# Kernel optimization log

Hardware: AMD Instinct MI355X
Metric: run time of the kernel (lower is better)

Reference implementation:

```python
import jax, jax.numpy as jnp
import numpy as np
import math

DIM_IN = 512
DIM_OUT = 512
KERNEL = 3
STYLE_DIM = 2 * 128
LIN_SCALE = 1.0 / math.sqrt(STYLE_DIM)      # EqualLinear scale (lr_mul=1)
CONV_SCALE = 1.0 / math.sqrt(DIM_IN * KERNEL ** 2)  # fan_in = dim_in * k**2 (as in source)
PAD = KERNEL // 2


def setup_inputs() -> dict:
    key = jax.random.key(0)
    ks = jax.random.split(key, 5)
    B, T = 16, 2048
    x = jax.random.normal(ks[0], (B, DIM_IN, T), dtype=jnp.float32)
    c_src = jax.random.normal(ks[1], (B, 128), dtype=jnp.float32)
    c_trg = jax.random.normal(ks[2], (B, 128), dtype=jnp.float32)
    style_w = jax.random.normal(ks[3], (DIM_IN, STYLE_DIM), dtype=jnp.float32)
    style_b = jnp.ones((DIM_IN,), dtype=jnp.float32)  # bias_init=1
    weight = jax.random.normal(ks[4], (1, DIM_OUT, DIM_IN, KERNEL), dtype=jnp.float32)
    return {"x": x, "c_src": c_src, "c_trg": c_trg,
            "style_w": style_w, "style_b": style_b, "weight": weight}


def reference(x, c_src, c_trg, style_w, style_b, weight):
    B = x.shape[0]
    # EqualLinear: style code s [B, dim_in]
    c = jnp.concatenate([c_src, c_trg], axis=-1)              # [B, 256]
    s = c @ (style_w * LIN_SCALE).T + style_b                 # [B, dim_in]
    # Modulate: w [B, dim_out, dim_in, k]
    w = CONV_SCALE * weight * s[:, None, :, None]
    # Demodulate over (dim_in, k)
    demod = jax.lax.rsqrt(jnp.sum(w * w, axis=(2, 3)) + 1e-8)  # [B, dim_out]
    w = w * demod[:, :, None, None]
    # Per-sample conv1d, padding 'same' (pad = k//2), vmapped over batch
    def conv1(xi, wi):
        # xi: [dim_in, T], wi: [dim_out, dim_in, k]
        out = jax.lax.conv_general_dilated(
            xi[None], wi, window_strides=(1,), padding=[(PAD, PAD)],
            dimension_numbers=("NCH", "OIH", "NCH"))
        return out[0]                                          # [dim_out, T]
    return jax.vmap(conv1)(x, w)                               # [B, dim_out, T]
```

## Files before the change

kernel.cpp:

```cpp
#include <hip/hip_runtime.h>
#include <cstdint>
#include <cstddef>


#define LIN_SCALE  0.0625f
#define CONV_SCALE 0.014731391f

#define B_   16
#define CIN  512
#define COUT 512
#define T_   2048
#define TP   2050

typedef __bf16 bf16x8 __attribute__((ext_vector_type(8)));
typedef float  f32x4  __attribute__((ext_vector_type(4)));

__device__ inline unsigned short f2bf(float f) {
  __bf16 h = (__bf16)f;
  return __builtin_bit_cast(unsigned short, h);
}

__global__ void style_kernel(const float* __restrict__ c_src,
                             const float* __restrict__ c_trg,
                             const float* __restrict__ sw,
                             const float* __restrict__ sb,
                             float* __restrict__ s) {
  __shared__ float c[256];
  const int b = blockIdx.x;
  const int tid = threadIdx.x;
  if (tid < 128)       c[tid] = c_src[b * 128 + tid];
  else if (tid < 256)  c[tid] = c_trg[b * 128 + tid - 128];
  __syncthreads();
  float acc = 0.f;
  const float* row = sw + (size_t)tid * 256;
  #pragma unroll 8
  for (int j = 0; j < 256; ++j) acc += row[j] * c[j];
  s[b * 512 + tid] = acc * LIN_SCALE + sb[tid];
}

__global__ __launch_bounds__(256) void modw_kernel(const float* __restrict__ weight,
                                                   const float* __restrict__ s,
                                                   unsigned short* __restrict__ Wm) {
  const int o = blockIdx.x, b = blockIdx.y;
  const int tid = threadIdx.x;
  __shared__ float sv[512];
  __shared__ float red[5];
  sv[tid]       = s[b * 512 + tid];
  sv[tid + 256] = s[b * 512 + tid + 256];
  __syncthreads();

  const float* wrow = weight + (size_t)o * 1536 + tid * 6;
  const int i0 = 2 * tid;
  float v[6]; float ss = 0.f;
  #pragma unroll
  for (int q = 0; q < 6; ++q) {
    const int i = i0 + (q >= 3);
    const float w = wrow[q] * CONV_SCALE * sv[i];
    v[q] = w; ss += w * w;
  }
  #pragma unroll
  for (int off = 32; off > 0; off >>= 1) ss += __shfl_down(ss, off, 64);
  if ((tid & 63) == 0) red[tid >> 6] = ss;
  __syncthreads();
  if (tid == 0) red[4] = rsqrtf(red[0] + red[1] + red[2] + red[3] + 1e-8f);
  __syncthreads();
  const float dem = red[4];

  #pragma unroll
  for (int q = 0; q < 6; ++q) {
    const int i = i0 + (q >= 3);
    const int k = (q >= 3) ? (q - 3) : q;
    Wm[(((size_t)b * 3 + k) * 512 + o) * 512 + i] = f2bf(v[q] * dem);
  }
}

__global__ __launch_bounds__(256) void transpose_kernel(const float* __restrict__ x,
                                                        unsigned short* __restrict__ xT) {
  __shared__ float tile[64][65];
  const int b = blockIdx.z, i0 = blockIdx.y * 64, t0 = blockIdx.x * 64;
  const int c  = threadIdx.x & 63;
  const int r0 = threadIdx.x >> 6;
  const float* xb = x + ((size_t)b * CIN + i0) * T_ + t0;
  #pragma unroll
  for (int rr = 0; rr < 64; rr += 4) {
    const int r = rr + r0;
    tile[r][c] = xb[(size_t)r * T_ + c];
  }
  __syncthreads();
  unsigned short* xTb = xT + ((size_t)b * TP + 1 + t0) * CIN + i0;
  #pragma unroll
  for (int rr = 0; rr < 64; rr += 4) {
    const int t = rr + r0;
    xTb[(size_t)t * CIN + c] = f2bf(tile[c][t]);
  }
}

__global__ void zpad_kernel(unsigned short* __restrict__ xT) {
  const int b = blockIdx.x;
  const size_t base = (size_t)b * TP * CIN;
  for (int j = threadIdx.x; j < CIN; j += 256) {
    xT[base + j] = 0;
    xT[base + (size_t)(TP - 1) * CIN + j] = 0;
  }
}

#define BM 128
#define BN 128
#define BK 64

__global__ __launch_bounds__(256, 2) void gemm_kernel(const unsigned short* __restrict__ Wm,
                                                      const unsigned short* __restrict__ xT,
                                                      float* __restrict__ out) {
  __shared__ unsigned short lA[BM * BK];
  __shared__ unsigned short lB[BN * BK];

  const int b  = blockIdx.z;
  const int o0 = blockIdx.y * BM;
  const int t0 = blockIdx.x * BN;
  const int tid  = threadIdx.x;
  const int lane = tid & 63;
  const int wm = (threadIdx.x >> 6 & 1) * 64;
  const int wn = (threadIdx.x >> 7) * 64;

  const int srow = tid >> 3;
  const int scol = (tid & 7) * 8;
  const unsigned short* gW = Wm + (size_t)b * 3 * 512 * 512 + (size_t)(o0 + srow) * 512 + scol;
  const unsigned short* gX = xT + (size_t)b * TP * CIN + (size_t)(t0 + srow) * CIN + scol;
  unsigned short* lAp = &lA[tid * 8];
  unsigned short* lBp = &lB[tid * 8];

  f32x4 acc[4][4];
  #pragma unroll
  for (int i = 0; i < 4; ++i)
    #pragma unroll
    for (int j = 0; j < 4; ++j) acc[i][j] = (f32x4){0.f, 0.f, 0.f, 0.f};

  for (int kk = 0; kk < 24; ++kk) {
    const int tap = kk >> 3;
    const int i0  = (kk & 7) * 64;
    const size_t offA = (size_t)tap * 512 * 512 + i0;
    const size_t offX = (size_t)tap * CIN + i0;
    __syncthreads();
    #pragma unroll
    for (int p = 0; p < 4; ++p)
      __builtin_amdgcn_global_load_lds(
          (const __attribute__((address_space(1))) void*)(gW + offA + (size_t)p * 32 * 512),
          (__attribute__((address_space(3))) void*)(lAp + p * 2048), 16, 0, 0);
    #pragma unroll
    for (int p = 0; p < 4; ++p)
      __builtin_amdgcn_global_load_lds(
          (const __attribute__((address_space(1))) void*)(gX + offX + (size_t)p * 32 * CIN),
          (__attribute__((address_space(3))) void*)(lBp + p * 2048), 16, 0, 0);
    __syncthreads();

    #pragma unroll
    for (int s = 0; s < 2; ++s) {
      const int ko = s * 32 + (lane >> 4) * 8;
      bf16x8 af[4], bfr[4];
      #pragma unroll
      for (int mi = 0; mi < 4; ++mi)
        af[mi] = *(const bf16x8*)&lA[(wm + mi * 16 + (lane & 15)) * BK + ko];
      #pragma unroll
      for (int ni = 0; ni < 4; ++ni)
        bfr[ni] = *(const bf16x8*)&lB[(wn + ni * 16 + (lane & 15)) * BK + ko];
      #pragma unroll
      for (int mi = 0; mi < 4; ++mi)
        #pragma unroll
        for (int ni = 0; ni < 4; ++ni)
          acc[mi][ni] = __builtin_amdgcn_mfma_f32_16x16x32_bf16(af[mi], bfr[ni], acc[mi][ni], 0, 0, 0);
    }
  }

  float* ob = out + ((size_t)b * COUT + o0 + wm) * T_ + t0 + wn;
  const int rrow = (lane >> 4) * 4;
  const int ccol = lane & 15;
  #pragma unroll
  for (int mi = 0; mi < 4; ++mi)
    #pragma unroll
    for (int ni = 0; ni < 4; ++ni)
      #pragma unroll
      for (int r = 0; r < 4; ++r)
        ob[(size_t)(mi * 16 + rrow + r) * T_ + ni * 16 + ccol] = acc[mi][ni][r];
}

extern "C" void kernel_launch(void* const* d_in, const int* in_sizes, int n_in,
                              void* d_out, int out_size, void* d_ws, size_t ws_size,
                              hipStream_t stream) {
  const float* x       = (const float*)d_in[0];
  const float* c_src   = (const float*)d_in[1];
  const float* c_trg   = (const float*)d_in[2];
  const float* style_w = (const float*)d_in[3];
  const float* style_b = (const float*)d_in[4];
  const float* weight  = (const float*)d_in[5];
  float* out = (float*)d_out;

  char* ws = (char*)d_ws;
  float* s_buf          = (float*)ws;
  unsigned short* Wm    = (unsigned short*)(ws + 32768);
  unsigned short* xTbuf = (unsigned short*)(ws + 32768 + 25165824);

  style_kernel<<<dim3(B_), 512, 0, stream>>>(c_src, c_trg, style_w, style_b, s_buf);
  modw_kernel<<<dim3(COUT, B_), 256, 0, stream>>>(weight, s_buf, Wm);
  transpose_kernel<<<dim3(T_ / 64, CIN / 64, B_), 256, 0, stream>>>(x, xTbuf);
  zpad_kernel<<<dim3(B_), 256, 0, stream>>>(xTbuf);
  gemm_kernel<<<dim3(T_ / BN, COUT / BM, B_), 256, 0, stream>>>(Wm, xTbuf, out);
}
```

Before: 211.9 us.

## Vectorize transpose, batch modulation across samples, parallelize style, raise GEMM occupancy

The style linear is spread over more blocks, with one wavefront reduction per output row. The modulation kernel now loads each weight row once and processes all 16 batch samples in that block, writing bf16 pairs. The transpose uses float4 loads and 16-byte bf16 stores, replacing scalar 2-byte stores. The GEMM launch bound is raised to 4 blocks per CU, which may force register spilling of the 64-float accumulator set.

```diff
diff --git a/kernel.cpp b/kernel.cpp
--- a/kernel.cpp
+++ b/kernel.cpp
@@ -14,63 +14,94 @@
 
 typedef __bf16 bf16x8 __attribute__((ext_vector_type(8)));
 typedef float  f32x4  __attribute__((ext_vector_type(4)));
+typedef unsigned short u16x8 __attribute__((ext_vector_type(8)));
+typedef unsigned short u16x2 __attribute__((ext_vector_type(2)));
 
 __device__ inline unsigned short f2bf(float f) {
   __bf16 h = (__bf16)f;
   return __builtin_bit_cast(unsigned short, h);
 }
 
-__global__ void style_kernel(const float* __restrict__ c_src,
-                             const float* __restrict__ c_trg,
-                             const float* __restrict__ sw,
-                             const float* __restrict__ sb,
-                             float* __restrict__ s) {
+__global__ __launch_bounds__(256) void style_kernel(const float* __restrict__ c_src,
+                                                    const float* __restrict__ c_trg,
+                                                    const float* __restrict__ sw,
+                                                    const float* __restrict__ sb,
+                                                    float* __restrict__ s) {
   __shared__ float c[256];
-  const int b = blockIdx.x;
+  const int b = blockIdx.y;
   const int tid = threadIdx.x;
-  if (tid < 128)       c[tid] = c_src[b * 128 + tid];
-  else if (tid < 256)  c[tid] = c_trg[b * 128 + tid - 128];
-  __syncthreads();
-  float acc = 0.f;
-  const float* row = sw + (size_t)tid * 256;
-  #pragma unroll 8
-  for (int j = 0; j < 256; ++j) acc += row[j] * c[j];
-  s[b * 512 + tid] = acc * LIN_SCALE + sb[tid];
+  c[tid] = (tid < 128) ? c_src[b * 128 + tid] : c_trg[b * 128 + tid - 128];
+  __syncthreads();
+  const int w = tid >> 6, lane = tid & 63;
+  #pragma unroll
+  for (int rr = 0; rr < 16; ++rr) {
+    const int i = blockIdx.x * 64 + w * 16 + rr;
+    const float* row = sw + (size_t)i * 256;
+    float acc = row[lane] * c[lane] + row[lane + 64] * c[lane + 64]
+              + row[lane + 128] * c[lane + 128] + row[lane + 192] * c[lane + 192];
+    #pragma unroll
+    for (int off = 32; off; off >>= 1) acc += __shfl_down(acc, off, 64);
+    if (lane == 0) s[b * 512 + i] = acc * LIN_SCALE + sb[i];
+  }
 }
 
 __global__ __launch_bounds__(256) void modw_kernel(const float* __restrict__ weight,
                                                    const float* __restrict__ s,
                                                    unsigned short* __restrict__ Wm) {
-  const int o = blockIdx.x, b = blockIdx.y;
+  const int o = blockIdx.x;
   const int tid = threadIdx.x;
-  __shared__ float sv[512];
-  __shared__ float red[5];
-  sv[tid]       = s[b * 512 + tid];
-  sv[tid + 256] = s[b * 512 + tid + 256];
-  __syncthreads();
-
-  const float* wrow = weight + (size_t)o * 1536 + tid * 6;
-  const int i0 = 2 * tid;
-  float v[6]; float ss = 0.f;
-  #pragma unroll
-  for (int q = 0; q < 6; ++q) {
-    const int i = i0 + (q >= 3);
-    const float w = wrow[q] * CONV_SCALE * sv[i];
-    v[q] = w; ss += w * w;
-  }
-  #pragma unroll
-  for (int off = 32; off > 0; off >>= 1) ss += __shfl_down(ss, off, 64);
-  if ((tid & 63) == 0) red[tid >> 6] = ss;
-  __syncthreads();
-  if (tid == 0) red[4] = rsqrtf(red[0] + red[1] + red[2] + red[3] + 1e-8f);
-  __syncthreads();
-  const float dem = red[4];
-
-  #pragma unroll
-  for (int q = 0; q < 6; ++q) {
-    const int i = i0 + (q >= 3);
-    const int k = (q >= 3) ? (q - 3) : q;
-    Wm[(((size_t)b * 3 + k) * 512 + o) * 512 + i] = f2bf(v[q] * dem);
+  __shared__ float wsh[1536];
+  __shared__ float svs[16 * 512];
+  __shared__ float partial[16][4];
+  __shared__ float demv[16];
+
+  #pragma unroll
+  for (int j = tid; j < 1536; j += 256) wsh[j] = weight[(size_t)o * 1536 + j];
+  #pragma unroll
+  for (int j = tid; j < 16 * 512; j += 256) svs[j] = s[j];
+  __syncthreads();
+
+  float wr[6];
+  #pragma unroll
+  for (int q = 0; q < 6; ++q) wr[q] = wsh[tid * 6 + q] * CONV_SCALE;
+
+  const int lane = tid & 63, w = tid >> 6;
+  float ssb[16];
+  #pragma unroll
+  for (int b = 0; b < 16; ++b) {
+    const float s0 = svs[b * 512 + 2 * tid];
+    const float s1 = svs[b * 512 + 2 * tid + 1];
+    float ss = 0.f;
+    #pragma unroll
+    for (int q = 0; q < 3; ++q) { float v = wr[q] * s0;     ss += v * v; }
+    #pragma unroll
+    for (int q = 3; q < 6; ++q) { float v = wr[q] * s1;     ss += v * v; }
+    ssb[b] = ss;
+  }
+  #pragma unroll
+  for (int b = 0; b < 16; ++b) {
+    float ss = ssb[b];
+    #pragma unroll
+    for (int off = 32; off; off >>= 1) ss += __shfl_down(ss, off, 64);
+    if (lane == 0) partial[b][w] = ss;
+  }
+  __syncthreads();
+  if (tid < 16)
+    demv[tid] = rsqrtf(partial[tid][0] + partial[tid][1] + partial[tid][2] + partial[tid][3] + 1e-8f);
+  __syncthreads();
+
+  #pragma unroll
+  for (int b = 0; b < 16; ++b) {
+    const float dem = demv[b];
+    const float s0 = svs[b * 512 + 2 * tid] * dem;
+    const float s1 = svs[b * 512 + 2 * tid + 1] * dem;
+    #pragma unroll
+    for (int k = 0; k < 3; ++k) {
+      u16x2 v;
+      v.x = f2bf(wr[k] * s0);
+      v.y = f2bf(wr[3 + k] * s1);
+      *(u16x2*)&Wm[(((size_t)b * 3 + k) * 512 + o) * 512 + 2 * tid] = v;
+    }
   }
 }
 
@@ -78,20 +109,30 @@
                                                         unsigned short* __restrict__ xT) {
   __shared__ float tile[64][65];
   const int b = blockIdx.z, i0 = blockIdx.y * 64, t0 = blockIdx.x * 64;
-  const int c  = threadIdx.x & 63;
-  const int r0 = threadIdx.x >> 6;
+  const int tid = threadIdx.x;
+
+  const int lr = tid >> 4;
+  const int lc = (tid & 15) * 4;
   const float* xb = x + ((size_t)b * CIN + i0) * T_ + t0;
   #pragma unroll
-  for (int rr = 0; rr < 64; rr += 4) {
-    const int r = rr + r0;
-    tile[r][c] = xb[(size_t)r * T_ + c];
-  }
-  __syncthreads();
+  for (int p = 0; p < 4; ++p) {
+    const int r = p * 16 + lr;
+    const float4 v = *(const float4*)(xb + (size_t)r * T_ + lc);
+    tile[r][lc + 0] = v.x; tile[r][lc + 1] = v.y;
+    tile[r][lc + 2] = v.z; tile[r][lc + 3] = v.w;
+  }
+  __syncthreads();
+
+  const int st = tid >> 3;
+  const int si = (tid & 7) * 8;
   unsigned short* xTb = xT + ((size_t)b * TP + 1 + t0) * CIN + i0;
   #pragma unroll
-  for (int rr = 0; rr < 64; rr += 4) {
-    const int t = rr + r0;
-    xTb[(size_t)t * CIN + c] = f2bf(tile[c][t]);
+  for (int p = 0; p < 2; ++p) {
+    const int t = p * 32 + st;
+    u16x8 v;
+    #pragma unroll
+    for (int q = 0; q < 8; ++q) v[q] = f2bf(tile[si + q][t]);
+    *(u16x8*)&xTb[(size_t)t * CIN + si] = v;
   }
 }
 
@@ -108,7 +149,7 @@
 #define BN 128
 #define BK 64
 
-__global__ __launch_bounds__(256, 2) void gemm_kernel(const unsigned short* __restrict__ Wm,
+__global__ __launch_bounds__(256, 4) void gemm_kernel(const unsigned short* __restrict__ Wm,
                                                       const unsigned short* __restrict__ xT,
                                                       float* __restrict__ out) {
   __shared__ unsigned short lA[BM * BK];
@@ -199,8 +240,8 @@
   unsigned short* Wm    = (unsigned short*)(ws + 32768);
   unsigned short* xTbuf = (unsigned short*)(ws + 32768 + 25165824);
 
-  style_kernel<<<dim3(B_), 512, 0, stream>>>(c_src, c_trg, style_w, style_b, s_buf);
-  modw_kernel<<<dim3(COUT, B_), 256, 0, stream>>>(weight, s_buf, Wm);
+  style_kernel<<<dim3(8, 16), 256, 0, stream>>>(c_src, c_trg, style_w, style_b, s_buf);
+  modw_kernel<<<dim3(COUT), 256, 0, stream>>>(weight, s_buf, Wm);
   transpose_kernel<<<dim3(T_ / 64, CIN / 64, B_), 256, 0, stream>>>(x, xTbuf);
   zpad_kernel<<<dim3(B_), 256, 0, stream>>>(xTbuf);
   gemm_kernel<<<dim3(T_ / BN, COUT / BM, B_), 256, 0, stream>>>(Wm, xTbuf, out);
```

Result: no change. 212.4 us (+0.2%).
